# Optimization experiments

Hardware: AMD Instinct MI355X
Metric: run time of the kernel (lower is better)

The kernel has to match this reference:

```python
import jax, jax.numpy as jnp
import numpy as np

RADIUS = 64
STRIDE = RADIUS // 2
EPS = 1e-5

def box_filter(x, w):
    # depthwise conv: groups=3, RADIUSxRADIUS kernel of ones, stride RADIUS//2, no padding
    return jax.lax.conv_general_dilated(
        x, w, window_strides=(STRIDE, STRIDE), padding='VALID',
        feature_group_count=3, dimension_numbers=('NCHW', 'OIHW', 'NCHW'))

def conv1x1(x, w):
    # 1x1 conv == per-pixel matmul over channels
    return jnp.einsum('bchw,oc->bohw', x, w)

def batchnorm(x, g, b):
    # BatchNorm2d in training mode: biased batch stats over (N,H,W)
    m = jnp.mean(x, axis=(0, 2, 3), keepdims=True)
    v = jnp.var(x, axis=(0, 2, 3), keepdims=True)
    return (x - m) * jax.lax.rsqrt(v + EPS) * g[None, :, None, None] + b[None, :, None, None]

def resize_bilinear_ac(x, oh, ow):
    # F.interpolate(mode='bilinear', align_corners=True), separable gathers
    B, C, h, w = x.shape
    ys = jnp.linspace(0.0, h - 1.0, oh)
    y0 = jnp.floor(ys).astype(jnp.int32)
    y1 = jnp.minimum(y0 + 1, h - 1)
    wy = (ys - y0.astype(x.dtype))[None, None, :, None]
    xh = jnp.take(x, y0, axis=2) * (1 - wy) + jnp.take(x, y1, axis=2) * wy
    xs = jnp.linspace(0.0, w - 1.0, ow)
    x0 = jnp.floor(xs).astype(jnp.int32)
    x1 = jnp.minimum(x0 + 1, w - 1)
    wx = (xs - x0.astype(x.dtype))[None, None, None, :]
    return jnp.take(xh, x0, axis=3) * (1 - wx) + jnp.take(xh, x1, axis=3) * wx

def setup_inputs():
    key = jax.random.key(0)
    ks = jax.random.split(key, 5)
    B, H, W = 4, 1024, 1024
    guide = jax.random.uniform(ks[0], (B, 3, H, W), dtype=jnp.float32)
    src = jax.random.uniform(ks[1], (B, 3, H, W), dtype=jnp.float32)
    box_w = jnp.ones((3, 1, RADIUS, RADIUS), jnp.float32)  # weight.data[...] = 1.0
    w1 = jax.random.normal(ks[2], (32, 6), jnp.float32) * 0.2
    w2 = jax.random.normal(ks[3], (32, 32), jnp.float32) * 0.2
    w3 = jax.random.normal(ks[4], (3, 32), jnp.float32) * 0.2
    g1 = jnp.ones((32,), jnp.float32); b1 = jnp.zeros((32,), jnp.float32)
    g2 = jnp.ones((32,), jnp.float32); b2 = jnp.zeros((32,), jnp.float32)
    return dict(guide=guide, src=src, box_w=box_w, w1=w1, g1=g1, b1=b1,
                w2=w2, g2=g2, b2=b2, w3=w3)

def reference(guide, src, box_w, w1, g1, b1, w2, g2, b2, w3):
    B, C, H, W = guide.shape
    N = box_filter(jnp.ones((1, 3, H, W), guide.dtype), box_w)  # local window counts
    mean_x = box_filter(guide, box_w) / N
    mean_y = box_filter(src, box_w) / N
    cov_xy = box_filter(guide * src, box_w) / N - mean_x * mean_y
    var_x = box_filter(guide * guide, box_w) / N - mean_x * mean_x
    h = jnp.concatenate([cov_xy, var_x], axis=1)  # [B,6,h',w']
    h = jax.nn.relu(batchnorm(conv1x1(h, w1), g1, b1))
    h = jax.nn.relu(batchnorm(conv1x1(h, w2), g2, b2))
    A = conv1x1(h, w3)  # [B,3,h',w']
    b = mean_y - A * mean_x
    mean_A = resize_bilinear_ac(A, H, W)
    mean_b = resize_bilinear_ac(b, H, W)
    return mean_A * guide + mean_b
```

## Files before the change

### kernel.cpp

```cpp
#include <hip/hip_runtime.h>
#include <stdint.h>

#define B_      4
#define C_      3
#define H_      1024
#define W_      1024
#define OH_     31
#define NHS_    64
#define NP_     3844
#define NPOSPB_ 961
#define EPS_    1e-5f

#define NBLK_    256
#define NTHR_    768
#define NSHARD_  8
#define SHARD_TGT_ 32
#define LINE_    32
#define NSHADOW_ 8

#define TILE_PLANE 24576
#define OFF_TILE  0
#define OFF_STATS 98304
#define OFF_A     99328
#define OFF_BV    110860

typedef float f4 __attribute__((ext_vector_type(4)));

__device__ int g_b0s[2][NSHARD_ * LINE_]; __device__ int g_b0r[2][LINE_];
__device__ int g_b1s[2][NSHARD_ * LINE_]; __device__ int g_b1r[2][LINE_];
__device__ int g_b2s[2][NSHARD_ * LINE_]; __device__ int g_b2r[2][LINE_];
__device__ int g_b3s[2][NSHARD_ * LINE_]; __device__ int g_b3r[2][LINE_];
__device__ int g_parity;

static __device__ __forceinline__ int  rload(int* p) { return __hip_atomic_load(p, __ATOMIC_RELAXED, __HIP_MEMORY_SCOPE_AGENT); }
static __device__ __forceinline__ int  aacq(int* p)  { return __hip_atomic_load(p, __ATOMIC_ACQUIRE, __HIP_MEMORY_SCOPE_AGENT); }
static __device__ __forceinline__ int  aadd(int* p, int v) { return __hip_atomic_fetch_add(p, v, __ATOMIC_ACQ_REL, __HIP_MEMORY_SCOPE_AGENT); }
static __device__ __forceinline__ void astoref(float* p, float v) { __hip_atomic_store(p, v, __ATOMIC_RELAXED, __HIP_MEMORY_SCOPE_AGENT); }
static __device__ __forceinline__ void astorei(int* p, int v)     { __hip_atomic_store(p, v, __ATOMIC_RELAXED, __HIP_MEMORY_SCOPE_AGENT); }
static __device__ __forceinline__ float aloadf(float* p) { return __hip_atomic_load(p, __ATOMIC_RELAXED, __HIP_MEMORY_SCOPE_AGENT); }

#define ARRIVE(shard, root) do { \
    if (t == 0) { \
        int _o = aadd(&(shard)[(fb & (NSHARD_ - 1)) * LINE_], 1); \
        if (_o == SHARD_TGT_ - 1) aadd(&(root)[0], 1); \
    } \
} while (0)
#define SPINROOT(root, slp) do { \
    if (t == 0) { \
        while (rload(&(root)[0]) < NSHARD_) __builtin_amdgcn_s_sleep(slp); \
        (void)aacq(&(root)[0]); \
    } \
    __syncthreads(); \
} while (0)

__global__ __launch_bounds__(NTHR_) void fused(
        const float* __restrict__ g,
        const float* __restrict__ s,
        const float* __restrict__ w1f,
        const float* __restrict__ g1f,
        const float* __restrict__ b1f,
        const float* __restrict__ w2f,
        const float* __restrict__ g2f,
        const float* __restrict__ b2f,
        const float* __restrict__ w3f,
        float* __restrict__ ws,
        float* __restrict__ out) {
    __shared__ float w1L[192];
    __shared__ float w2L[32 * 33];
    __shared__ float w3L[3 * 33];
    __shared__ float Sarr[16][12];
    __shared__ float hbuf[16][8];
    __shared__ float mxb[16][4], myb[16][4];
    __shared__ float sbuf[16][33];
    __shared__ float zbuf[16][33];
    __shared__ float scs[32], shs[32];
    __shared__ int sP;
    int t  = threadIdx.x;
    int fb = blockIdx.x;
    if (t == 0) sP = rload(&g_parity);

    if (t < 192) w1L[t] = w1f[t];
    for (int i = t; i < 1024; i += NTHR_) w2L[(i >> 5) * 33 + (i & 31)] = w2f[i];
    if (t < 96) w3L[(t >> 5) * 33 + (t & 31)] = w3f[t];

    int sub = t >> 8;
    int st  = t & 255;
    f4 gvals[16];
    {
        int unit = fb * 3 + sub;
        int ibc = unit >> 6, hs = unit & 63;
        const f4* gp = (const f4*)(g + ((size_t)ibc * H_ + (size_t)hs * 16) * W_);
        const f4* sp = (const f4*)(s + ((size_t)ibc * H_ + (size_t)hs * 16) * W_);
        float sg = 0.f, ss = 0.f, sgs = 0.f, sgg = 0.f;
#pragma unroll
        for (int r = 0; r < 16; r++) {
            f4 gv = __builtin_nontemporal_load(gp + r * (W_ / 4) + st);
            f4 sv = __builtin_nontemporal_load(sp + r * (W_ / 4) + st);
            gvals[r] = gv;
            sg  += (gv.x + gv.y) + (gv.z + gv.w);
            ss  += (sv.x + sv.y) + (sv.z + sv.w);
            sgs += gv.x * sv.x + gv.y * sv.y + gv.z * sv.z + gv.w * sv.w;
            sgg += gv.x * gv.x + gv.y * gv.y + gv.z * gv.z + gv.w * gv.w;
        }
#pragma unroll
        for (int off = 4; off; off >>= 1) {
            sg  += __shfl_down(sg,  off, 8);
            ss  += __shfl_down(ss,  off, 8);
            sgs += __shfl_down(sgs, off, 8);
            sgg += __shfl_down(sgg, off, 8);
        }
        if ((st & 7) == 0) {
            int tx = st >> 3;
            int base = (ibc * NHS_ + hs) * 32 + tx;
            astoref(&ws[OFF_TILE + 0 * TILE_PLANE + base], sg);
            astoref(&ws[OFF_TILE + 1 * TILE_PLANE + base], ss);
            astoref(&ws[OFF_TILE + 2 * TILE_PLANE + base], sgs);
            astoref(&ws[OFF_TILE + 3 * TILE_PLANE + base], sgg);
        }
        if (fb == 0) for (int i = t; i < NSHADOW_ * 128; i += NTHR_) astoref(&ws[OFF_STATS + i], 0.f);
    }
    __syncthreads();
    int P = sP;
    ARRIVE(g_b0s[P], g_b0r[P]);

    SPINROOT(g_b0r[P], 2);

    int p0 = fb * 16;
    if (t < 192) {
        int ipos = t / 12, idx = t % 12;
        int c = idx >> 2, plane = idx & 3;
        int p = p0 + ipos; if (p >= NP_) p = 0;
        int b = p / NPOSPB_, r = p % NPOSPB_;
        int oy = r / OH_, ox = r % OH_;
        const float* tp = ws + OFF_TILE + plane * TILE_PLANE + ((b * 3 + c) * NHS_ + oy * 2) * 32 + ox;
        Sarr[ipos][idx] = ((tp[0]  + tp[1])  + (tp[32] + tp[33]))
                        + ((tp[64] + tp[65]) + (tp[96] + tp[97]));
    }
    __syncthreads();
    if (t < 48) {
        int pos = t / 3, c = t % 3;
        const float inv = 1.f / 4096.f;
        float mx = Sarr[pos][c * 4 + 0] * inv, my = Sarr[pos][c * 4 + 1] * inv;
        hbuf[pos][c]     = Sarr[pos][c * 4 + 2] * inv - mx * my;
        hbuf[pos][3 + c] = Sarr[pos][c * 4 + 3] * inv - mx * mx;
        mxb[pos][c] = mx; myb[pos][c] = my;
    }
    __syncthreads();
    int pos = t >> 5, ch = t & 31;
    bool act = t < 512;
    bool valid = act && (p0 + pos) < NP_;
    float y1 = 0.f;
    if (act) {
#pragma unroll
        for (int i = 0; i < 6; i++) y1 += w1L[ch * 6 + i] * hbuf[pos][i];
        sbuf[pos][ch] = valid ? y1 : 0.f;
    }
    __syncthreads();
    if (t < 32) {
        float sv = 0.f, sq = 0.f;
#pragma unroll
        for (int i = 0; i < 16; i++) { float v = sbuf[i][t]; sv += v; sq += v * v; }
        float* sh0 = ws + OFF_STATS + (fb & (NSHADOW_ - 1)) * 128;
        atomicAdd(&sh0[t], sv); atomicAdd(&sh0[32 + t], sq);
    }
    __syncthreads();
    ARRIVE(g_b1s[P], g_b1r[P]);
    SPINROOT(g_b1r[P], 2);
    if (t < 32) {
        float sm = 0.f, sq = 0.f;
#pragma unroll
        for (int k = 0; k < NSHADOW_; k++) {
            sm += aloadf(&ws[OFF_STATS + k * 128 + t]);
            sq += aloadf(&ws[OFF_STATS + k * 128 + 32 + t]);
        }
        float m = sm * (1.f / NP_);
        float v = sq * (1.f / NP_) - m * m;
        float sc = g1f[t] * rsqrtf(v + EPS_);
        scs[t] = sc; shs[t] = b1f[t] - m * sc;
    }
    __syncthreads();
    if (act) zbuf[pos][ch] = fmaxf(y1 * scs[ch] + shs[ch], 0.f);
    __syncthreads();
    float y2 = 0.f;
    if (act) {
#pragma unroll
        for (int i = 0; i < 32; i++) y2 += w2L[ch * 33 + i] * zbuf[pos][i];
        sbuf[pos][ch] = valid ? y2 : 0.f;
    }
    __syncthreads();
    if (t < 32) {
        float sv = 0.f, sq = 0.f;
#pragma unroll
        for (int i = 0; i < 16; i++) { float v = sbuf[i][t]; sv += v; sq += v * v; }
        float* sh0 = ws + OFF_STATS + (fb & (NSHADOW_ - 1)) * 128;
        atomicAdd(&sh0[64 + t], sv); atomicAdd(&sh0[96 + t], sq);
    }
    __syncthreads();
    ARRIVE(g_b2s[P], g_b2r[P]);
    SPINROOT(g_b2r[P], 2);
    if (t < 32) {
        float sm = 0.f, sq = 0.f;
#pragma unroll
        for (int k = 0; k < NSHADOW_; k++) {
            sm += aloadf(&ws[OFF_STATS + k * 128 + 64 + t]);
            sq += aloadf(&ws[OFF_STATS + k * 128 + 96 + t]);
        }
        float m = sm * (1.f / NP_);
        float v = sq * (1.f / NP_) - m * m;
        float sc = g2f[t] * rsqrtf(v + EPS_);
        scs[t] = sc; shs[t] = b2f[t] - m * sc;
    }
    __syncthreads();
    if (act) zbuf[pos][ch] = fmaxf(y2 * scs[ch] + shs[ch], 0.f);
    __syncthreads();
    if (t < 48) {
        int pz = t / 3, c = t % 3;
        int p = p0 + pz;
        if (p < NP_) {
            float A = 0.f;
#pragma unroll
            for (int i = 0; i < 32; i++) A += w3L[c * 33 + i] * zbuf[pz][i];
            astoref(&ws[OFF_A  + c * NP_ + p], A);
            astoref(&ws[OFF_BV + c * NP_ + p], myb[pz][c] - A * mxb[pz][c]);
        }
    }
    __syncthreads();
    if (t == 0) {
        int old = aadd(&g_b3s[P][(fb & (NSHARD_ - 1)) * LINE_], 1);
        if (old == SHARD_TGT_ - 1) {
            int ro = aadd(&g_b3r[P][0], 1);
            if (ro == NSHARD_ - 1) {
                int Q = P ^ 1;
#pragma unroll
                for (int i = 0; i < NSHARD_; i++) {
                    astorei(&g_b0s[Q][i * LINE_], 0); astorei(&g_b1s[Q][i * LINE_], 0);
                    astorei(&g_b2s[Q][i * LINE_], 0); astorei(&g_b3s[Q][i * LINE_], 0);
                }
                astorei(&g_b0r[Q][0], 0); astorei(&g_b1r[Q][0], 0);
                astorei(&g_b2r[Q][0], 0); astorei(&g_b3r[Q][0], 0);
                __hip_atomic_store(&g_parity, Q, __ATOMIC_RELEASE, __HIP_MEMORY_SCOPE_AGENT);
            }
        }
    }
    SPINROOT(g_b3r[P], 8);

    {
        int row0 = fb * 48 + sub * 16;
        int bc = row0 >> 10;
        int b5 = bc / 3, c5 = bc % 3;
        const float* Abase = ws + OFF_A  + c5 * NP_ + b5 * NPOSPB_;
        const float* Bbase = ws + OFF_BV + c5 * NP_ + b5 * NPOSPB_;
        int x0_[4], x1_[4]; float wx_[4];
#pragma unroll
        for (int j = 0; j < 4; j++) {
            int x = st * 4 + j;
            float fx = (float)x * (30.f / 1023.f);
            int x0 = (int)fx;
            wx_[j] = fx - (float)x0;
            x0_[j] = x0;
            x1_[j] = min(x0 + 1, 30);
        }
#pragma unroll
        for (int rr = 0; rr < 16; rr++) {
            int y = (row0 & 1023) + rr;
            float fy = (float)y * (30.f / 1023.f);
            int y0 = (int)fy;
            float wy = fy - (float)y0;
            int y1i = min(y0 + 1, 30);
            const float* A0 = Abase + y0  * OH_;
            const float* A1 = Abase + y1i * OH_;
            const float* B0 = Bbase + y0  * OH_;
            const float* B1 = Bbase + y1i * OH_;
            size_t rowoff = ((size_t)bc * H_ + (size_t)y) * W_;
            f4 gv = gvals[rr];
            float go[4] = { gv.x, gv.y, gv.z, gv.w };
            float r[4];
#pragma unroll
            for (int j = 0; j < 4; j++) {
                int x0 = x0_[j], x1 = x1_[j];
                float wx = wx_[j];
                float av = (A0[x0] * (1.f - wx) + A0[x1] * wx) * (1.f - wy)
                         + (A1[x0] * (1.f - wx) + A1[x1] * wx) * wy;
                float bb = (B0[x0] * (1.f - wx) + B0[x1] * wx) * (1.f - wy)
                         + (B1[x0] * (1.f - wx) + B1[x1] * wx) * wy;
                r[j] = av * go[j] + bb;
            }
            f4 ov; ov.x = r[0]; ov.y = r[1]; ov.z = r[2]; ov.w = r[3];
            __builtin_nontemporal_store(ov, (f4*)(out + rowoff) + st);
        }
    }
}

extern "C" void kernel_launch(void* const* d_in, const int* in_sizes, int n_in,
                              void* d_out, int out_size, void* d_ws, size_t ws_size,
                              hipStream_t stream) {
    const float* guide = (const float*)d_in[0];
    const float* src   = (const float*)d_in[1];
    const float* w1 = (const float*)d_in[3];
    const float* g1 = (const float*)d_in[4];
    const float* b1 = (const float*)d_in[5];
    const float* w2 = (const float*)d_in[6];
    const float* g2 = (const float*)d_in[7];
    const float* b2 = (const float*)d_in[8];
    const float* w3 = (const float*)d_in[9];
    float* ws = (float*)d_ws;
    float* out = (float*)d_out;

    hipLaunchKernelGGL(fused, dim3(NBLK_), dim3(NTHR_), 0, stream,
                       guide, src, w1, g1, b1, w2, g2, b2, w3, ws, out);
}
```

Measured before the change: 198.9 us.

## Split persistent fused kernel into three launches with grid barriers only for BN stats

Replaces the single persistent kernel, which used four software grid barriers, with three kernels. The first computes tile sums, the second is a 128-block, 1024-thread kernel that keeps grid barriers only for the two batchnorm reductions, and the third is a row-per-block bilinear upsample and output kernel. Kernel boundaries take the place of the first and last grid barriers. The cost is that the final pass must re-read the guide from memory instead of reusing guide values held in registers, and there are extra launch overheads.

```diff
diff --git a/kernel.cpp b/kernel.cpp
--- a/kernel.cpp
+++ b/kernel.cpp
@@ -11,10 +11,9 @@
 #define NPOSPB_ 961
 #define EPS_    1e-5f
 
-#define NBLK_    256
-#define NTHR_    768
+#define NBLK2_   128
 #define NSHARD_  8
-#define SHARD_TGT_ 32
+#define SHARD_TGT_ 16
 #define LINE_    32
 #define NSHADOW_ 8
 
@@ -26,36 +25,55 @@
 
 typedef float f4 __attribute__((ext_vector_type(4)));
 
-__device__ int g_b0s[2][NSHARD_ * LINE_]; __device__ int g_b0r[2][LINE_];
 __device__ int g_b1s[2][NSHARD_ * LINE_]; __device__ int g_b1r[2][LINE_];
 __device__ int g_b2s[2][NSHARD_ * LINE_]; __device__ int g_b2r[2][LINE_];
-__device__ int g_b3s[2][NSHARD_ * LINE_]; __device__ int g_b3r[2][LINE_];
 __device__ int g_parity;
 
 static __device__ __forceinline__ int  rload(int* p) { return __hip_atomic_load(p, __ATOMIC_RELAXED, __HIP_MEMORY_SCOPE_AGENT); }
 static __device__ __forceinline__ int  aacq(int* p)  { return __hip_atomic_load(p, __ATOMIC_ACQUIRE, __HIP_MEMORY_SCOPE_AGENT); }
 static __device__ __forceinline__ int  aadd(int* p, int v) { return __hip_atomic_fetch_add(p, v, __ATOMIC_ACQ_REL, __HIP_MEMORY_SCOPE_AGENT); }
-static __device__ __forceinline__ void astoref(float* p, float v) { __hip_atomic_store(p, v, __ATOMIC_RELAXED, __HIP_MEMORY_SCOPE_AGENT); }
-static __device__ __forceinline__ void astorei(int* p, int v)     { __hip_atomic_store(p, v, __ATOMIC_RELAXED, __HIP_MEMORY_SCOPE_AGENT); }
+static __device__ __forceinline__ void astorei(int* p, int v) { __hip_atomic_store(p, v, __ATOMIC_RELAXED, __HIP_MEMORY_SCOPE_AGENT); }
 static __device__ __forceinline__ float aloadf(float* p) { return __hip_atomic_load(p, __ATOMIC_RELAXED, __HIP_MEMORY_SCOPE_AGENT); }
 
-#define ARRIVE(shard, root) do { \
-    if (t == 0) { \
-        int _o = aadd(&(shard)[(fb & (NSHARD_ - 1)) * LINE_], 1); \
-        if (_o == SHARD_TGT_ - 1) aadd(&(root)[0], 1); \
-    } \
-} while (0)
-#define SPINROOT(root, slp) do { \
-    if (t == 0) { \
-        while (rload(&(root)[0]) < NSHARD_) __builtin_amdgcn_s_sleep(slp); \
-        (void)aacq(&(root)[0]); \
-    } \
-    __syncthreads(); \
-} while (0)
-
-__global__ __launch_bounds__(NTHR_) void fused(
+__global__ __launch_bounds__(256) void k1_tilesums(
         const float* __restrict__ g,
         const float* __restrict__ s,
+        float* __restrict__ ws) {
+    int blk = blockIdx.x;
+    int bc = blk >> 6;
+    int hs = blk & 63;
+    int t  = threadIdx.x;
+    const f4* gp = (const f4*)(g + ((size_t)bc * H_ + (size_t)hs * 16) * W_);
+    const f4* sp = (const f4*)(s + ((size_t)bc * H_ + (size_t)hs * 16) * W_);
+    float sg = 0.f, ss = 0.f, sgs = 0.f, sgg = 0.f;
+#pragma unroll 4
+    for (int r = 0; r < 16; r++) {
+        f4 gv = gp[r * (W_ / 4) + t];
+        f4 sv = __builtin_nontemporal_load(sp + r * (W_ / 4) + t);
+        sg  += (gv.x + gv.y) + (gv.z + gv.w);
+        ss  += (sv.x + sv.y) + (sv.z + sv.w);
+        sgs += gv.x * sv.x + gv.y * sv.y + gv.z * sv.z + gv.w * sv.w;
+        sgg += gv.x * gv.x + gv.y * gv.y + gv.z * gv.z + gv.w * gv.w;
+    }
+#pragma unroll
+    for (int off = 4; off; off >>= 1) {
+        sg  += __shfl_down(sg,  off, 8);
+        ss  += __shfl_down(ss,  off, 8);
+        sgs += __shfl_down(sgs, off, 8);
+        sgg += __shfl_down(sgg, off, 8);
+    }
+    if ((t & 7) == 0) {
+        int tx = t >> 3;
+        int base = (bc * NHS_ + hs) * 32 + tx;
+        ws[OFF_TILE + 0 * TILE_PLANE + base] = sg;
+        ws[OFF_TILE + 1 * TILE_PLANE + base] = ss;
+        ws[OFF_TILE + 2 * TILE_PLANE + base] = sgs;
+        ws[OFF_TILE + 3 * TILE_PLANE + base] = sgg;
+    }
+    if (blk == 0) for (int i = t; i < NSHADOW_ * 128; i += 256) ws[OFF_STATS + i] = 0.f;
+}
+
+__global__ __launch_bounds__(1024) void kmid(
         const float* __restrict__ w1f,
         const float* __restrict__ g1f,
         const float* __restrict__ b1f,
@@ -63,16 +81,15 @@
         const float* __restrict__ g2f,
         const float* __restrict__ b2f,
         const float* __restrict__ w3f,
-        float* __restrict__ ws,
-        float* __restrict__ out) {
+        float* __restrict__ ws) {
     __shared__ float w1L[192];
     __shared__ float w2L[32 * 33];
     __shared__ float w3L[3 * 33];
-    __shared__ float Sarr[16][12];
-    __shared__ float hbuf[16][8];
-    __shared__ float mxb[16][4], myb[16][4];
-    __shared__ float sbuf[16][33];
-    __shared__ float zbuf[16][33];
+    __shared__ float Sarr[32][12];
+    __shared__ float hbuf[32][8];
+    __shared__ float mxb[32][4], myb[32][4];
+    __shared__ float sbuf[32][33];
+    __shared__ float zbuf[32][33];
     __shared__ float scs[32], shs[32];
     __shared__ int sP;
     int t  = threadIdx.x;
@@ -80,53 +97,11 @@
     if (t == 0) sP = rload(&g_parity);
 
     if (t < 192) w1L[t] = w1f[t];
-    for (int i = t; i < 1024; i += NTHR_) w2L[(i >> 5) * 33 + (i & 31)] = w2f[i];
-    if (t < 96) w3L[(t >> 5) * 33 + (t & 31)] = w3f[t];
-
-    int sub = t >> 8;
-    int st  = t & 255;
-    f4 gvals[16];
-    {
-        int unit = fb * 3 + sub;
-        int ibc = unit >> 6, hs = unit & 63;
-        const f4* gp = (const f4*)(g + ((size_t)ibc * H_ + (size_t)hs * 16) * W_);
-        const f4* sp = (const f4*)(s + ((size_t)ibc * H_ + (size_t)hs * 16) * W_);
-        float sg = 0.f, ss = 0.f, sgs = 0.f, sgg = 0.f;
-#pragma unroll
-        for (int r = 0; r < 16; r++) {
-            f4 gv = __builtin_nontemporal_load(gp + r * (W_ / 4) + st);
-            f4 sv = __builtin_nontemporal_load(sp + r * (W_ / 4) + st);
-            gvals[r] = gv;
-            sg  += (gv.x + gv.y) + (gv.z + gv.w);
-            ss  += (sv.x + sv.y) + (sv.z + sv.w);
-            sgs += gv.x * sv.x + gv.y * sv.y + gv.z * sv.z + gv.w * sv.w;
-            sgg += gv.x * gv.x + gv.y * gv.y + gv.z * gv.z + gv.w * gv.w;
-        }
-#pragma unroll
-        for (int off = 4; off; off >>= 1) {
-            sg  += __shfl_down(sg,  off, 8);
-            ss  += __shfl_down(ss,  off, 8);
-            sgs += __shfl_down(sgs, off, 8);
-            sgg += __shfl_down(sgg, off, 8);
-        }
-        if ((st & 7) == 0) {
-            int tx = st >> 3;
-            int base = (ibc * NHS_ + hs) * 32 + tx;
-            astoref(&ws[OFF_TILE + 0 * TILE_PLANE + base], sg);
-            astoref(&ws[OFF_TILE + 1 * TILE_PLANE + base], ss);
-            astoref(&ws[OFF_TILE + 2 * TILE_PLANE + base], sgs);
-            astoref(&ws[OFF_TILE + 3 * TILE_PLANE + base], sgg);
-        }
-        if (fb == 0) for (int i = t; i < NSHADOW_ * 128; i += NTHR_) astoref(&ws[OFF_STATS + i], 0.f);
-    }
-    __syncthreads();
-    int P = sP;
-    ARRIVE(g_b0s[P], g_b0r[P]);
-
-    SPINROOT(g_b0r[P], 2);
-
-    int p0 = fb * 16;
-    if (t < 192) {
+    w2L[(t >> 5) * 33 + (t & 31)] = w2f[t];
+    if (t >= 256 && t < 352) { int i = t - 256; w3L[(i / 32) * 33 + (i & 31)] = w3f[i]; }
+
+    int p0 = fb * 32;
+    if (t < 384) {
         int ipos = t / 12, idx = t % 12;
         int c = idx >> 2, plane = idx & 3;
         int p = p0 + ipos; if (p >= NP_) p = 0;
@@ -137,7 +112,7 @@
                         + ((tp[64] + tp[65]) + (tp[96] + tp[97]));
     }
     __syncthreads();
-    if (t < 48) {
+    if (t < 96) {
         int pos = t / 3, c = t % 3;
         const float inv = 1.f / 4096.f;
         float mx = Sarr[pos][c * 4 + 0] * inv, my = Sarr[pos][c * 4 + 1] * inv;
@@ -147,25 +122,28 @@
     }
     __syncthreads();
     int pos = t >> 5, ch = t & 31;
-    bool act = t < 512;
-    bool valid = act && (p0 + pos) < NP_;
+    bool valid = (p0 + pos) < NP_;
     float y1 = 0.f;
-    if (act) {
-#pragma unroll
-        for (int i = 0; i < 6; i++) y1 += w1L[ch * 6 + i] * hbuf[pos][i];
-        sbuf[pos][ch] = valid ? y1 : 0.f;
-    }
+#pragma unroll
+    for (int i = 0; i < 6; i++) y1 += w1L[ch * 6 + i] * hbuf[pos][i];
+    sbuf[pos][ch] = valid ? y1 : 0.f;
     __syncthreads();
     if (t < 32) {
         float sv = 0.f, sq = 0.f;
 #pragma unroll
-        for (int i = 0; i < 16; i++) { float v = sbuf[i][t]; sv += v; sq += v * v; }
+        for (int i = 0; i < 32; i++) { float v = sbuf[i][t]; sv += v; sq += v * v; }
         float* sh0 = ws + OFF_STATS + (fb & (NSHADOW_ - 1)) * 128;
         atomicAdd(&sh0[t], sv); atomicAdd(&sh0[32 + t], sq);
     }
     __syncthreads();
-    ARRIVE(g_b1s[P], g_b1r[P]);
-    SPINROOT(g_b1r[P], 2);
+    int P = sP;
+    if (t == 0) {
+        int o = aadd(&g_b1s[P][(fb & (NSHARD_ - 1)) * LINE_], 1);
+        if (o == SHARD_TGT_ - 1) aadd(&g_b1r[P][0], 1);
+        while (rload(&g_b1r[P][0]) < NSHARD_) __builtin_amdgcn_s_sleep(4);
+        (void)aacq(&g_b1r[P][0]);
+    }
+    __syncthreads();
     if (t < 32) {
         float sm = 0.f, sq = 0.f;
 #pragma unroll
@@ -179,25 +157,41 @@
         scs[t] = sc; shs[t] = b1f[t] - m * sc;
     }
     __syncthreads();
-    if (act) zbuf[pos][ch] = fmaxf(y1 * scs[ch] + shs[ch], 0.f);
+    zbuf[pos][ch] = fmaxf(y1 * scs[ch] + shs[ch], 0.f);
     __syncthreads();
     float y2 = 0.f;
-    if (act) {
-#pragma unroll
-        for (int i = 0; i < 32; i++) y2 += w2L[ch * 33 + i] * zbuf[pos][i];
-        sbuf[pos][ch] = valid ? y2 : 0.f;
-    }
+#pragma unroll
+    for (int i = 0; i < 32; i++) y2 += w2L[ch * 33 + i] * zbuf[pos][i];
+    sbuf[pos][ch] = valid ? y2 : 0.f;
     __syncthreads();
     if (t < 32) {
         float sv = 0.f, sq = 0.f;
 #pragma unroll
-        for (int i = 0; i < 16; i++) { float v = sbuf[i][t]; sv += v; sq += v * v; }
+        for (int i = 0; i < 32; i++) { float v = sbuf[i][t]; sv += v; sq += v * v; }
         float* sh0 = ws + OFF_STATS + (fb & (NSHADOW_ - 1)) * 128;
         atomicAdd(&sh0[64 + t], sv); atomicAdd(&sh0[96 + t], sq);
     }
     __syncthreads();
-    ARRIVE(g_b2s[P], g_b2r[P]);
-    SPINROOT(g_b2r[P], 2);
+    if (t == 0) {
+        int o = aadd(&g_b2s[P][(fb & (NSHARD_ - 1)) * LINE_], 1);
+        if (o == SHARD_TGT_ - 1) {
+            int ro = aadd(&g_b2r[P][0], 1);
+            if (ro == NSHARD_ - 1) {
+                int Q = P ^ 1;
+#pragma unroll
+                for (int i = 0; i < NSHARD_; i++) {
+                    astorei(&g_b1s[Q][i * LINE_], 0);
+                    astorei(&g_b2s[Q][i * LINE_], 0);
+                }
+                astorei(&g_b1r[Q][0], 0);
+                astorei(&g_b2r[Q][0], 0);
+                __hip_atomic_store(&g_parity, Q, __ATOMIC_RELEASE, __HIP_MEMORY_SCOPE_AGENT);
+            }
+        }
+        while (rload(&g_b2r[P][0]) < NSHARD_) __builtin_amdgcn_s_sleep(4);
+        (void)aacq(&g_b2r[P][0]);
+    }
+    __syncthreads();
     if (t < 32) {
         float sm = 0.f, sq = 0.f;
 #pragma unroll
@@ -211,84 +205,60 @@
         scs[t] = sc; shs[t] = b2f[t] - m * sc;
     }
     __syncthreads();
-    if (act) zbuf[pos][ch] = fmaxf(y2 * scs[ch] + shs[ch], 0.f);
-    __syncthreads();
-    if (t < 48) {
+    zbuf[pos][ch] = fmaxf(y2 * scs[ch] + shs[ch], 0.f);
+    __syncthreads();
+    if (t < 96) {
         int pz = t / 3, c = t % 3;
         int p = p0 + pz;
         if (p < NP_) {
             float A = 0.f;
 #pragma unroll
             for (int i = 0; i < 32; i++) A += w3L[c * 33 + i] * zbuf[pz][i];
-            astoref(&ws[OFF_A  + c * NP_ + p], A);
-            astoref(&ws[OFF_BV + c * NP_ + p], myb[pz][c] - A * mxb[pz][c]);
-        }
-    }
-    __syncthreads();
-    if (t == 0) {
-        int old = aadd(&g_b3s[P][(fb & (NSHARD_ - 1)) * LINE_], 1);
-        if (old == SHARD_TGT_ - 1) {
-            int ro = aadd(&g_b3r[P][0], 1);
-            if (ro == NSHARD_ - 1) {
-                int Q = P ^ 1;
-#pragma unroll
-                for (int i = 0; i < NSHARD_; i++) {
-                    astorei(&g_b0s[Q][i * LINE_], 0); astorei(&g_b1s[Q][i * LINE_], 0);
-                    astorei(&g_b2s[Q][i * LINE_], 0); astorei(&g_b3s[Q][i * LINE_], 0);
-                }
-                astorei(&g_b0r[Q][0], 0); astorei(&g_b1r[Q][0], 0);
-                astorei(&g_b2r[Q][0], 0); astorei(&g_b3r[Q][0], 0);
-                __hip_atomic_store(&g_parity, Q, __ATOMIC_RELEASE, __HIP_MEMORY_SCOPE_AGENT);
-            }
-        }
-    }
-    SPINROOT(g_b3r[P], 8);
-
-    {
-        int row0 = fb * 48 + sub * 16;
-        int bc = row0 >> 10;
-        int b5 = bc / 3, c5 = bc % 3;
-        const float* Abase = ws + OFF_A  + c5 * NP_ + b5 * NPOSPB_;
-        const float* Bbase = ws + OFF_BV + c5 * NP_ + b5 * NPOSPB_;
-        int x0_[4], x1_[4]; float wx_[4];
-#pragma unroll
-        for (int j = 0; j < 4; j++) {
-            int x = st * 4 + j;
-            float fx = (float)x * (30.f / 1023.f);
-            int x0 = (int)fx;
-            wx_[j] = fx - (float)x0;
-            x0_[j] = x0;
-            x1_[j] = min(x0 + 1, 30);
-        }
-#pragma unroll
-        for (int rr = 0; rr < 16; rr++) {
-            int y = (row0 & 1023) + rr;
-            float fy = (float)y * (30.f / 1023.f);
-            int y0 = (int)fy;
-            float wy = fy - (float)y0;
-            int y1i = min(y0 + 1, 30);
-            const float* A0 = Abase + y0  * OH_;
-            const float* A1 = Abase + y1i * OH_;
-            const float* B0 = Bbase + y0  * OH_;
-            const float* B1 = Bbase + y1i * OH_;
-            size_t rowoff = ((size_t)bc * H_ + (size_t)y) * W_;
-            f4 gv = gvals[rr];
-            float go[4] = { gv.x, gv.y, gv.z, gv.w };
-            float r[4];
-#pragma unroll
-            for (int j = 0; j < 4; j++) {
-                int x0 = x0_[j], x1 = x1_[j];
-                float wx = wx_[j];
-                float av = (A0[x0] * (1.f - wx) + A0[x1] * wx) * (1.f - wy)
-                         + (A1[x0] * (1.f - wx) + A1[x1] * wx) * wy;
-                float bb = (B0[x0] * (1.f - wx) + B0[x1] * wx) * (1.f - wy)
-                         + (B1[x0] * (1.f - wx) + B1[x1] * wx) * wy;
-                r[j] = av * go[j] + bb;
-            }
-            f4 ov; ov.x = r[0]; ov.y = r[1]; ov.z = r[2]; ov.w = r[3];
-            __builtin_nontemporal_store(ov, (f4*)(out + rowoff) + st);
-        }
-    }
+            ws[OFF_A  + c * NP_ + p] = A;
+            ws[OFF_BV + c * NP_ + p] = myb[pz][c] - A * mxb[pz][c];
+        }
+    }
+}
+
+__global__ __launch_bounds__(256) void k5_final(
+        const float* __restrict__ g,
+        const float* __restrict__ ws,
+        float* __restrict__ out) {
+    int blk = blockIdx.x;
+    int y  = blk & 1023;
+    int bc = blk >> 10;
+    int b = bc / 3, c = bc % 3;
+    float fy = (float)y * (30.f / 1023.f);
+    int y0 = (int)fy;
+    float wy = fy - (float)y0;
+    int y1i = min(y0 + 1, 30);
+    const float* A0 = ws + OFF_A  + c * NP_ + b * NPOSPB_ + y0  * OH_;
+    const float* A1 = ws + OFF_A  + c * NP_ + b * NPOSPB_ + y1i * OH_;
+    const float* B0 = ws + OFF_BV + c * NP_ + b * NPOSPB_ + y0  * OH_;
+    const float* B1 = ws + OFF_BV + c * NP_ + b * NPOSPB_ + y1i * OH_;
+    int t = threadIdx.x;
+    size_t rowoff = ((size_t)bc * H_ + (size_t)y) * W_;
+    const f4* gp = (const f4*)(g + rowoff);
+    f4* op = (f4*)(out + rowoff);
+    f4 gv = gp[t];
+    float go[4] = { gv.x, gv.y, gv.z, gv.w };
+    float r[4];
+#pragma unroll
+    for (int j = 0; j < 4; j++) {
+        int x = t * 4 + j;
+        float fx = (float)x * (30.f / 1023.f);
+        int x0 = (int)fx;
+        float wx = fx - (float)x0;
+        int x1 = min(x0 + 1, 30);
+        float a  = (A0[x0] * (1.f - wx) + A0[x1] * wx) * (1.f - wy)
+                 + (A1[x0] * (1.f - wx) + A1[x1] * wx) * wy;
+        float bb = (B0[x0] * (1.f - wx) + B0[x1] * wx) * (1.f - wy)
+                 + (B1[x0] * (1.f - wx) + B1[x1] * wx) * wy;
+        r[j] = a * go[j] + bb;
+    }
+    f4 ov;
+    ov.x = r[0]; ov.y = r[1]; ov.z = r[2]; ov.w = r[3];
+    __builtin_nontemporal_store(ov, op + t);
 }
 
 extern "C" void kernel_launch(void* const* d_in, const int* in_sizes, int n_in,
@@ -306,6 +276,8 @@
     float* ws = (float*)d_ws;
     float* out = (float*)d_out;
 
-    hipLaunchKernelGGL(fused, dim3(NBLK_), dim3(NTHR_), 0, stream,
-                       guide, src, w1, g1, b1, w2, g2, b2, w3, ws, out);
-}
+    hipLaunchKernelGGL(k1_tilesums, dim3(B_ * C_ * NHS_), dim3(256),  0, stream, guide, src, ws);
+    hipLaunchKernelGGL(kmid,        dim3(NBLK2_),         dim3(1024), 0, stream,
+                       w1, g1, b1, w2, g2, b2, w3, ws);
+    hipLaunchKernelGGL(k5_final,    dim3(B_ * C_ * H_),   dim3(256),  0, stream, guide, ws, out);
+}
```

Result: faster. 175.0 us (-12.0%).
